# Kernel tuning notes

Hardware: AMD Instinct MI355X
Metric: run time of the kernel (lower is better)

Reference implementation:

```python
import jax, jax.numpy as jnp
import numpy as np


def setup_inputs() -> dict:
    key = jax.random.key(0)
    # D must equal N for the elementwise Multiply([inputs, attn]) to broadcast.
    B, N = 16, 1024
    x = jax.random.normal(key, (B, N, N), dtype=jnp.float32)
    return {"x": x}


def reference(x) -> jnp.ndarray:
    # scores[b,i,j] = <x[b,i,:], x[b,j,:]>  -> [B, N, N]
    scores = jnp.einsum("bid,bjd->bij", x, x)
    attn = jax.nn.softmax(scores, axis=-1)
    # NOTE: elementwise multiply (not a weighted sum) — faithful to the source.
    return x * attn
```

## Files before the change

### kernel.cpp

```cpp
#include <hip/hip_runtime.h>
#include <hip/hip_bf16.h>

#define BATCH   16
#define NN      1024
#define ROWS    64
#define NWAVES  16
#define NTHR    1024
#define NCT     4
#define MT      4

typedef __attribute__((ext_vector_type(8))) short short8;
typedef __attribute__((ext_vector_type(4))) float f32x4;

static __device__ __forceinline__ unsigned short cvt_bf16(float f) {
    unsigned int u = __builtin_bit_cast(unsigned int, f);
    u += 0x7fffu + ((u >> 16) & 1u);
    return (unsigned short)(u >> 16);
}

__global__ __launch_bounds__(256)
void cvt_kernel(const float* __restrict__ x, unsigned short* __restrict__ xw) {
    const int n4 = BATCH * NN * NN / 4;
    int i = blockIdx.x * 256 + threadIdx.x;
    const int stride = gridDim.x * 256;
    for (; i < n4; i += stride) {
        float4 v = reinterpret_cast<const float4*>(x)[i];
        ushort4 h;
        h.x = cvt_bf16(v.x); h.y = cvt_bf16(v.y);
        h.z = cvt_bf16(v.z); h.w = cvt_bf16(v.w);
        reinterpret_cast<ushort4*>(xw)[i] = h;
    }
}

__global__ __launch_bounds__(NTHR)
void attn_v3(const float* __restrict__ x, const unsigned short* __restrict__ xw,
             float* __restrict__ out) {
    const int wg   = blockIdx.x;
    const int t    = wg >> 3;
    const int b    = (wg & 7) + 8 * (t >> 4);
    const int i0   = (t & 15) * ROWS;
    const int tid  = threadIdx.x;
    const int lane = tid & 63;
    const int wid  = tid >> 6;
    const int l15  = lane & 15;
    const int g    = lane >> 4;

    const float* xb = x + (size_t)b * NN * NN;

    __shared__ unsigned short ldsA[ROWS * NN];
    __shared__ float redbuf[NWAVES][ROWS];

    {
        const unsigned short* Aw = xw + (size_t)b * NN * NN + (size_t)i0 * NN;
        #pragma unroll
        for (int it = 0; it < (ROWS * NN / 4) / NTHR; ++it) {
            int f4  = tid + it * NTHR;
            int row = f4 >> 8;
            int d   = (f4 & 255) << 2;
            ushort4 h = *reinterpret_cast<const ushort4*>(Aw + row * NN + d);
            int e = (row * NN + d) ^ ((row & 15) << 3);
            *reinterpret_cast<ushort4*>(&ldsA[e]) = h;
        }
    }
    __syncthreads();

    f32x4 acc[MT][NCT];
    #pragma unroll
    for (int r = 0; r < MT; ++r)
        #pragma unroll
        for (int ct = 0; ct < NCT; ++ct)
            acc[r][ct] = (f32x4){0.f, 0.f, 0.f, 0.f};

    const int jb = wid * (NCT * 16);
    const unsigned short* Bb = xw + (size_t)b * NN * NN
                                  + (size_t)(jb + l15) * NN + g * 8;

    #pragma unroll 1
    for (int k = 0; k < NN; k += 64) {
        short8 blo[NCT], bhi[NCT];
        #pragma unroll
        for (int ct = 0; ct < NCT; ++ct) {
            const unsigned short* p = Bb + ct * (16 * NN) + k;
            blo[ct] = *reinterpret_cast<const short8*>(p);
            bhi[ct] = *reinterpret_cast<const short8*>(p + 32);
        }
        __builtin_amdgcn_s_setprio(1);
        #pragma unroll
        for (int r = 0; r < MT; ++r) {
            const int base = (r * 16 + l15) * NN + g * 8;
            short8 a0 = *reinterpret_cast<const short8*>(
                            &ldsA[(base + k)      ^ (l15 << 3)]);
            short8 a1 = *reinterpret_cast<const short8*>(
                            &ldsA[(base + k + 32) ^ (l15 << 3)]);
            #pragma unroll
            for (int ct = 0; ct < NCT; ++ct) {
                acc[r][ct] = __builtin_amdgcn_mfma_f32_16x16x32_bf16(
                    a0, blo[ct], acc[r][ct], 0, 0, 0);
                acc[r][ct] = __builtin_amdgcn_mfma_f32_16x16x32_bf16(
                    a1, bhi[ct], acc[r][ct], 0, 0, 0);
            }
        }
        __builtin_amdgcn_s_setprio(0);
    }

    float mrow[MT][4];
    #pragma unroll
    for (int r = 0; r < MT; ++r)
        #pragma unroll
        for (int q = 0; q < 4; ++q) {
            float m = acc[r][0][q];
            #pragma unroll
            for (int ct = 1; ct < NCT; ++ct) m = fmaxf(m, acc[r][ct][q]);
            #pragma unroll
            for (int s = 1; s < 16; s <<= 1) m = fmaxf(m, __shfl_xor(m, s, 64));
            mrow[r][q] = m;
        }
    if (l15 == 0) {
        #pragma unroll
        for (int r = 0; r < MT; ++r)
            #pragma unroll
            for (int q = 0; q < 4; ++q)
                redbuf[wid][r * 16 + g * 4 + q] = mrow[r][q];
    }
    __syncthreads();
    #pragma unroll
    for (int r = 0; r < MT; ++r)
        #pragma unroll
        for (int q = 0; q < 4; ++q) {
            int row = r * 16 + g * 4 + q;
            float m = redbuf[0][row];
            #pragma unroll
            for (int w = 1; w < NWAVES; ++w) m = fmaxf(m, redbuf[w][row]);
            mrow[r][q] = m;
        }
    __syncthreads();

    float srow[MT][4];
    #pragma unroll
    for (int r = 0; r < MT; ++r)
        #pragma unroll
        for (int q = 0; q < 4; ++q) {
            float s = 0.f;
            #pragma unroll
            for (int ct = 0; ct < NCT; ++ct) {
                float e = __expf(acc[r][ct][q] - mrow[r][q]);
                acc[r][ct][q] = e;
                s += e;
            }
            #pragma unroll
            for (int sh = 1; sh < 16; sh <<= 1) s += __shfl_xor(s, sh, 64);
            srow[r][q] = s;
        }
    if (l15 == 0) {
        #pragma unroll
        for (int r = 0; r < MT; ++r)
            #pragma unroll
            for (int q = 0; q < 4; ++q)
                redbuf[wid][r * 16 + g * 4 + q] = srow[r][q];
    }
    __syncthreads();

    float* ob = out + (size_t)b * NN * NN;
    #pragma unroll
    for (int r = 0; r < MT; ++r)
        #pragma unroll
        for (int q = 0; q < 4; ++q) {
            int row = r * 16 + g * 4 + q;
            float tot = redbuf[0][row];
            #pragma unroll
            for (int w = 1; w < NWAVES; ++w) tot += redbuf[w][row];
            float inv = 1.0f / tot;
            const size_t rowoff = (size_t)(i0 + row) * NN;
            #pragma unroll
            for (int ct = 0; ct < NCT; ++ct) {
                int j_ = jb + ct * 16 + l15;
                ob[rowoff + j_] = xb[rowoff + j_] * acc[r][ct][q] * inv;
            }
        }
}

#define FB_NWAVES 8
#define FB_NTHR   512
#define FB_NCT    8

static __device__ __forceinline__ short8 cvt8(float4 u0, float4 u1) {
    short8 r;
    r[0] = (short)cvt_bf16(u0.x); r[1] = (short)cvt_bf16(u0.y);
    r[2] = (short)cvt_bf16(u0.z); r[3] = (short)cvt_bf16(u0.w);
    r[4] = (short)cvt_bf16(u1.x); r[5] = (short)cvt_bf16(u1.y);
    r[6] = (short)cvt_bf16(u1.z); r[7] = (short)cvt_bf16(u1.w);
    return r;
}

__global__ __launch_bounds__(FB_NTHR, 2)
void attn_fb(const float* __restrict__ x, float* __restrict__ out) {
    const int wg   = blockIdx.x;
    const int t    = wg >> 3;
    const int b    = (wg & 7) + 8 * (t >> 4);
    const int i0   = (t & 15) * ROWS;
    const int tid  = threadIdx.x;
    const int lane = tid & 63;
    const int wid  = tid >> 6;
    const int l15  = lane & 15;
    const int g    = lane >> 4;

    const float* xb = x + (size_t)b * NN * NN;
    __shared__ unsigned short ldsA[ROWS * NN];
    __shared__ float redbuf[FB_NWAVES][ROWS];

    {
        const float* Ar = xb + (size_t)i0 * NN;
        #pragma unroll
        for (int it = 0; it < (ROWS * NN / 4) / FB_NTHR; ++it) {
            int f4  = tid + it * FB_NTHR;
            int row = f4 >> 8;
            int d   = (f4 & 255) << 2;
            float4 v = *reinterpret_cast<const float4*>(Ar + row * NN + d);
            int e = (row * NN + d) ^ ((row & 15) << 3);
            ushort4 h;
            h.x = cvt_bf16(v.x); h.y = cvt_bf16(v.y);
            h.z = cvt_bf16(v.z); h.w = cvt_bf16(v.w);
            *reinterpret_cast<ushort4*>(&ldsA[e]) = h;
        }
    }
    __syncthreads();

    f32x4 acc[MT][FB_NCT];
    #pragma unroll
    for (int r = 0; r < MT; ++r)
        #pragma unroll
        for (int ct = 0; ct < FB_NCT; ++ct)
            acc[r][ct] = (f32x4){0.f, 0.f, 0.f, 0.f};

    const int jb = wid * (FB_NCT * 16);
    const float* Bb = xb + (size_t)(jb + l15) * NN + g * 8;

    #pragma unroll 1
    for (int k = 0; k < NN; k += 32) {
        short8 ar[MT];
        #pragma unroll
        for (int r = 0; r < MT; ++r) {
            int e = ((r * 16 + l15) * NN + k + g * 8) ^ (l15 << 3);
            ar[r] = *reinterpret_cast<const short8*>(&ldsA[e]);
        }
        #pragma unroll
        for (int ct = 0; ct < FB_NCT; ++ct) {
            const float* p = Bb + ct * (16 * NN) + k;
            float4 u0 = *reinterpret_cast<const float4*>(p);
            float4 u1 = *reinterpret_cast<const float4*>(p + 4);
            short8 bf = cvt8(u0, u1);
            #pragma unroll
            for (int r = 0; r < MT; ++r)
                acc[r][ct] = __builtin_amdgcn_mfma_f32_16x16x32_bf16(
                    ar[r], bf, acc[r][ct], 0, 0, 0);
        }
    }

    float mrow[MT][4];
    #pragma unroll
    for (int r = 0; r < MT; ++r)
        #pragma unroll
        for (int q = 0; q < 4; ++q) {
            float m = acc[r][0][q];
            #pragma unroll
            for (int ct = 1; ct < FB_NCT; ++ct) m = fmaxf(m, acc[r][ct][q]);
            #pragma unroll
            for (int s = 1; s < 16; s <<= 1) m = fmaxf(m, __shfl_xor(m, s, 64));
            mrow[r][q] = m;
        }
    if (l15 == 0) {
        #pragma unroll
        for (int r = 0; r < MT; ++r)
            #pragma unroll
            for (int q = 0; q < 4; ++q)
                redbuf[wid][r * 16 + g * 4 + q] = mrow[r][q];
    }
    __syncthreads();
    #pragma unroll
    for (int r = 0; r < MT; ++r)
        #pragma unroll
        for (int q = 0; q < 4; ++q) {
            int row = r * 16 + g * 4 + q;
            float m = redbuf[0][row];
            #pragma unroll
            for (int w = 1; w < FB_NWAVES; ++w) m = fmaxf(m, redbuf[w][row]);
            mrow[r][q] = m;
        }
    __syncthreads();

    float srow[MT][4];
    #pragma unroll
    for (int r = 0; r < MT; ++r)
        #pragma unroll
        for (int q = 0; q < 4; ++q) {
            float s = 0.f;
            #pragma unroll
            for (int ct = 0; ct < FB_NCT; ++ct) {
                float e = __expf(acc[r][ct][q] - mrow[r][q]);
                acc[r][ct][q] = e;
                s += e;
            }
            #pragma unroll
            for (int sh = 1; sh < 16; sh <<= 1) s += __shfl_xor(s, sh, 64);
            srow[r][q] = s;
        }
    if (l15 == 0) {
        #pragma unroll
        for (int r = 0; r < MT; ++r)
            #pragma unroll
            for (int q = 0; q < 4; ++q)
                redbuf[wid][r * 16 + g * 4 + q] = srow[r][q];
    }
    __syncthreads();

    float* ob = out + (size_t)b * NN * NN;
    #pragma unroll
    for (int r = 0; r < MT; ++r)
        #pragma unroll
        for (int q = 0; q < 4; ++q) {
            int row = r * 16 + g * 4 + q;
            float tot = redbuf[0][row];
            #pragma unroll
            for (int w = 1; w < FB_NWAVES; ++w) tot += redbuf[w][row];
            float inv = 1.0f / tot;
            const size_t rowoff = (size_t)(i0 + row) * NN;
            #pragma unroll
            for (int ct = 0; ct < FB_NCT; ++ct) {
                int j_ = jb + ct * 16 + l15;
                ob[rowoff + j_] = xb[rowoff + j_] * acc[r][ct][q] * inv;
            }
        }
}

extern "C" void kernel_launch(void* const* d_in, const int* in_sizes, int n_in,
                              void* d_out, int out_size, void* d_ws, size_t ws_size,
                              hipStream_t stream) {
    const float* x = (const float*)d_in[0];
    float* out = (float*)d_out;
    const size_t need = (size_t)BATCH * NN * NN * sizeof(unsigned short);
    dim3 grid(BATCH * (NN / ROWS));
    if (ws_size >= need) {
        unsigned short* xw = (unsigned short*)d_ws;
        cvt_kernel<<<2048, 256, 0, stream>>>(x, xw);
        attn_v3<<<grid, NTHR, 0, stream>>>(x, xw, out);
    } else {
        attn_fb<<<grid, FB_NTHR, 0, stream>>>(x, out);
    }
}
```

Before: 192.5 us.

## Double-buffer operand tiles in LDS via async global_load_lds and coalesce epilogue stores

Replaces the one-time A-tile preload plus per-lane strided global B loads with a K-stepped loop. Each step stages a 32-wide slice of all 1024 bf16 rows of the batch into one of two 64KB LDS buffers using asynchronous global_load_lds with an XOR swizzle, and prefetches the next slice while the current one feeds the MFMAs. The epilogue now transposes normalized probabilities through LDS so each wave writes full rows with float4 coalesced loads and stores. The cost is 128KB of LDS (one workgroup per CU), a barrier on every K step, and extra barriers in the epilogue.

```diff
diff --git a/kernel.cpp b/kernel.cpp
--- a/kernel.cpp
+++ b/kernel.cpp
@@ -6,8 +6,10 @@
 #define ROWS    64
 #define NWAVES  16
 #define NTHR    1024
+#define BK      32
+#define NSTEP   (NN / BK)
+#define MT      4
 #define NCT     4
-#define MT      4
 
 typedef __attribute__((ext_vector_type(8))) short short8;
 typedef __attribute__((ext_vector_type(4))) float f32x4;
@@ -32,37 +34,44 @@
     }
 }
 
-__global__ __launch_bounds__(NTHR)
-void attn_v3(const float* __restrict__ x, const unsigned short* __restrict__ xw,
+#define STAGE(bb, k0)                                                          \
+    {                                                                          \
+        _Pragma("unroll")                                                      \
+        for (int c = 0; c < 4; ++c) {                                          \
+            __builtin_amdgcn_global_load_lds(                                  \
+                (const __attribute__((address_space(1))) void*)(xwb + soff[c] + (k0)), \
+                (__attribute__((address_space(3))) void*)(lds + (bb) * 65536 + (wid * 4 + c) * 1024), \
+                16, 0, 0);                                                     \
+        }                                                                      \
+    }
+
+__global__ __launch_bounds__(NTHR, 1)
+void attn_v4(const float* __restrict__ x, const unsigned short* __restrict__ xw,
              float* __restrict__ out) {
     const int wg   = blockIdx.x;
-    const int t    = wg >> 3;
-    const int b    = (wg & 7) + 8 * (t >> 4);
-    const int i0   = (t & 15) * ROWS;
+    const int t_   = wg >> 3;
+    const int b    = (wg & 7) + 8 * (t_ >> 4);
+    const int i0   = (t_ & 15) * ROWS;
     const int tid  = threadIdx.x;
     const int lane = tid & 63;
     const int wid  = tid >> 6;
     const int l15  = lane & 15;
     const int g    = lane >> 4;
 
-    const float* xb = x + (size_t)b * NN * NN;
-
-    __shared__ unsigned short ldsA[ROWS * NN];
+    __shared__ __align__(16) unsigned char lds[131072];
     __shared__ float redbuf[NWAVES][ROWS];
 
-    {
-        const unsigned short* Aw = xw + (size_t)b * NN * NN + (size_t)i0 * NN;
-        #pragma unroll
-        for (int it = 0; it < (ROWS * NN / 4) / NTHR; ++it) {
-            int f4  = tid + it * NTHR;
-            int row = f4 >> 8;
-            int d   = (f4 & 255) << 2;
-            ushort4 h = *reinterpret_cast<const ushort4*>(Aw + row * NN + d);
-            int e = (row * NN + d) ^ ((row & 15) << 3);
-            *reinterpret_cast<ushort4*>(&ldsA[e]) = h;
-        }
-    }
-    __syncthreads();
+    const unsigned short* xwb = xw + (size_t)b * (NN * NN);
+    const float* xb = x + (size_t)b * (NN * NN);
+
+    int soff[4];
+    #pragma unroll
+    for (int c = 0; c < 4; ++c) {
+        int G   = wid * 256 + c * 64 + lane;
+        int row = G >> 2;
+        int sg  = (lane & 3) ^ ((row >> 1) & 3);
+        soff[c] = row * NN + sg * 8;
+    }
 
     f32x4 acc[MT][NCT];
     #pragma unroll
@@ -72,35 +81,39 @@
             acc[r][ct] = (f32x4){0.f, 0.f, 0.f, 0.f};
 
     const int jb = wid * (NCT * 16);
-    const unsigned short* Bb = xw + (size_t)b * NN * NN
-                                  + (size_t)(jb + l15) * NN + g * 8;
+
+    STAGE(0, 0)
+    __syncthreads();
 
     #pragma unroll 1
-    for (int k = 0; k < NN; k += 64) {
-        short8 blo[NCT], bhi[NCT];
+    for (int t = 0; t < NSTEP; ++t) {
+        if (t + 1 < NSTEP) STAGE((t + 1) & 1, (t + 1) * BK)
+
+        const unsigned char* cur = lds + (t & 1) * 65536;
+        short8 af[MT], bfr[NCT];
+        #pragma unroll
+        for (int r = 0; r < MT; ++r) {
+            int row = i0 + r * 16 + l15;
+            int gr  = row * 4 + (g ^ ((row >> 1) & 3));
+            af[r] = *reinterpret_cast<const short8*>(cur + gr * 16);
+        }
         #pragma unroll
         for (int ct = 0; ct < NCT; ++ct) {
-            const unsigned short* p = Bb + ct * (16 * NN) + k;
-            blo[ct] = *reinterpret_cast<const short8*>(p);
-            bhi[ct] = *reinterpret_cast<const short8*>(p + 32);
-        }
+            int row = jb + ct * 16 + l15;
+            int gr  = row * 4 + (g ^ ((row >> 1) & 3));
+            bfr[ct] = *reinterpret_cast<const short8*>(cur + gr * 16);
+        }
+
         __builtin_amdgcn_s_setprio(1);
         #pragma unroll
-        for (int r = 0; r < MT; ++r) {
-            const int base = (r * 16 + l15) * NN + g * 8;
-            short8 a0 = *reinterpret_cast<const short8*>(
-                            &ldsA[(base + k)      ^ (l15 << 3)]);
-            short8 a1 = *reinterpret_cast<const short8*>(
-                            &ldsA[(base + k + 32) ^ (l15 << 3)]);
-            #pragma unroll
-            for (int ct = 0; ct < NCT; ++ct) {
+        for (int r = 0; r < MT; ++r)
+            #pragma unroll
+            for (int ct = 0; ct < NCT; ++ct)
                 acc[r][ct] = __builtin_amdgcn_mfma_f32_16x16x32_bf16(
-                    a0, blo[ct], acc[r][ct], 0, 0, 0);
-                acc[r][ct] = __builtin_amdgcn_mfma_f32_16x16x32_bf16(
-                    a1, bhi[ct], acc[r][ct], 0, 0, 0);
-            }
-        }
+                    af[r], bfr[ct], acc[r][ct], 0, 0, 0);
         __builtin_amdgcn_s_setprio(0);
+
+        __syncthreads();
     }
 
     float mrow[MT][4];
@@ -135,7 +148,6 @@
         }
     __syncthreads();
 
-    float srow[MT][4];
     #pragma unroll
     for (int r = 0; r < MT; ++r)
         #pragma unroll
@@ -149,20 +161,15 @@
             }
             #pragma unroll
             for (int sh = 1; sh < 16; sh <<= 1) s += __shfl_xor(s, sh, 64);
-            srow[r][q] = s;
-        }
-    if (l15 == 0) {
-        #pragma unroll
-        for (int r = 0; r < MT; ++r)
-            #pragma unroll
-            for (int q = 0; q < 4; ++q)
-                redbuf[wid][r * 16 + g * 4 + q] = srow[r][q];
-    }
-    __syncthreads();
-
+            if (l15 == 0) redbuf[wid][r * 16 + g * 4 + q] = s;
+        }
+    __syncthreads();
+
+    float* Pb = (float*)lds;
     float* ob = out + (size_t)b * NN * NN;
     #pragma unroll
-    for (int r = 0; r < MT; ++r)
+    for (int r = 0; r < MT; ++r) {
+        __syncthreads();
         #pragma unroll
         for (int q = 0; q < 4; ++q) {
             int row = r * 16 + g * 4 + q;
@@ -170,13 +177,26 @@
             #pragma unroll
             for (int w = 1; w < NWAVES; ++w) tot += redbuf[w][row];
             float inv = 1.0f / tot;
-            const size_t rowoff = (size_t)(i0 + row) * NN;
-            #pragma unroll
-            for (int ct = 0; ct < NCT; ++ct) {
-                int j_ = jb + ct * 16 + l15;
-                ob[rowoff + j_] = xb[rowoff + j_] * acc[r][ct][q] * inv;
-            }
-        }
+            #pragma unroll
+            for (int ct = 0; ct < NCT; ++ct)
+                Pb[(g * 4 + q) * NN + (jb + ct * 16 + l15)] = acc[r][ct][q] * inv;
+        }
+        __syncthreads();
+        const int rowg   = i0 + r * 16 + wid;
+        const float* xr  = xb + (size_t)rowg * NN;
+        float*       orw = ob + (size_t)rowg * NN;
+        const float* pr  = Pb + wid * NN;
+        #pragma unroll
+        for (int jj = 0; jj < 4; ++jj) {
+            int cix = jj * 256 + lane * 4;
+            float4 pv = *reinterpret_cast<const float4*>(pr + cix);
+            float4 xv = *reinterpret_cast<const float4*>(xr + cix);
+            float4 ov;
+            ov.x = xv.x * pv.x; ov.y = xv.y * pv.y;
+            ov.z = xv.z * pv.z; ov.w = xv.w * pv.w;
+            *reinterpret_cast<float4*>(orw + cix) = ov;
+        }
+    }
 }
 
 #define FB_NWAVES 8
@@ -342,7 +362,7 @@
     if (ws_size >= need) {
         unsigned short* xw = (unsigned short*)d_ws;
         cvt_kernel<<<2048, 256, 0, stream>>>(x, xw);
-        attn_v3<<<grid, NTHR, 0, stream>>>(x, xw, out);
+        attn_v4<<<grid, NTHR, 0, stream>>>(x, xw, out);
     } else {
         attn_fb<<<grid, FB_NTHR, 0, stream>>>(x, out);
     }
```

Result: slower. 292.6 us (+52.0%).
